# Performance work log

Measured on AMD Instinct MI355X. Metric: run time of the kernel, lower is better.

## Reference

```python
import jax, jax.numpy as jnp
import numpy as np

HEADS = 16
EPS = 1e-6


def _layernorm(x, gamma, beta):
    # LayerNorm over the last dim (per-head channel dim), eps=1e-6, affine.
    mu = jnp.mean(x, axis=-1, keepdims=True)
    var = jnp.mean(jnp.square(x - mu), axis=-1, keepdims=True)
    return (x - mu) * jax.lax.rsqrt(var + EPS) * gamma + beta


def setup_inputs() -> dict:
    key = jax.random.key(0)
    k_qkv, = jax.random.split(key, 1)
    bs, n_ctx, width3 = 1, 4096, 3072  # packed qkv: 3 * model_width (model_width=1024)
    attn_ch = width3 // HEADS // 3     # 64
    qkv = jax.random.normal(k_qkv, (bs, n_ctx, width3), dtype=jnp.float32)
    return {
        "qkv": qkv,
        "q_gamma": jnp.ones((attn_ch,), dtype=jnp.float32),
        "q_beta": jnp.zeros((attn_ch,), dtype=jnp.float32),
        "k_gamma": jnp.ones((attn_ch,), dtype=jnp.float32),
        "k_beta": jnp.zeros((attn_ch,), dtype=jnp.float32),
    }


def reference(qkv, q_gamma, q_beta, k_gamma, k_beta):
    bs, n_ctx, width3 = qkv.shape
    attn_ch = width3 // HEADS // 3
    # scale applied to both q and k -> total 1/sqrt(attn_ch)
    scale = 1.0 / np.sqrt(np.sqrt(attn_ch))
    qkv = qkv.reshape(bs, n_ctx, HEADS, 3 * attn_ch)
    q, k, v = jnp.split(qkv, 3, axis=-1)  # each [b, n, h, c]
    q = _layernorm(q, q_gamma, q_beta)
    k = _layernorm(k, k_gamma, k_beta)
    # manual (flash=False) path: einsum -> fp32 softmax -> einsum
    weight = jnp.einsum('bthc,bshc->bhts', q * scale, k * scale)
    wdtype = weight.dtype
    weight = jax.nn.softmax(weight.astype(jnp.float32), axis=-1).astype(wdtype)
    out = jnp.einsum('bhts,bshc->bthc', weight, v).reshape(bs, n_ctx, HEADS * attn_ch)
    return out
```

## Files before the change

### kernel.cpp

```cpp
#include <hip/hip_runtime.h>
#include <math.h>

#define TCTX 4096
#define HEADS 16
#define W3 3072
#define BQ 128
#define BK 64
#define NT 512
#define LSTR 65
#define HSTR 72

typedef short bf16x8 __attribute__((ext_vector_type(8)));
typedef float f32x4 __attribute__((ext_vector_type(4)));

static __device__ __forceinline__ unsigned short f2bf(float x) {
    union { float f; unsigned int u; } v; v.f = x;
    unsigned int r = v.u + 0x7fffu + ((v.u >> 16) & 1u);
    return (unsigned short)(r >> 16);
}
static __device__ __forceinline__ float bf2f(unsigned short h) {
    union { float f; unsigned int u; } v; v.u = ((unsigned int)h) << 16;
    return v.f;
}
#define PK2(a,b) ((unsigned int)(a) | ((unsigned int)(b) << 16))

__global__ __launch_bounds__(NT, 1) void attn_r17_kernel(
    const float* __restrict__ qkv,
    const float* __restrict__ q_gamma, const float* __restrict__ q_beta,
    const float* __restrict__ k_gamma, const float* __restrict__ k_beta,
    float* __restrict__ out)
{
    __shared__ float Ss[BQ * LSTR];
    __shared__ unsigned short Qh[BQ * HSTR], Ql[BQ * HSTR];
    __shared__ unsigned short Kh[BK * HSTR], Kl[BK * HSTR];
    __shared__ unsigned short Vth[64 * HSTR], Vtl[64 * HSTR];
    __shared__ unsigned short Ph[BQ * HSTR], Pl[BQ * HSTR];
    __shared__ float axs[BQ];
    __shared__ float lin[BQ];

    const int tid  = threadIdx.x;
    const int h    = blockIdx.y;
    const int q0   = blockIdx.x * BQ;
    const int lane = tid & 63;
    const int wv   = tid >> 6;
    const int l15  = lane & 15;
    const int quad = lane >> 4;
    const int m0   = wv * 16;
    const int r    = tid >> 2;
    const int j    = tid & 3;

    const float scale = 0.35355339059327373f;

    {
        const float* qp = qkv + (size_t)(q0 + r) * W3 + h * 192 + j * 16;
        f32x4 x0 = *(const f32x4*)(qp);
        f32x4 x1 = *(const f32x4*)(qp + 4);
        f32x4 x2 = *(const f32x4*)(qp + 8);
        f32x4 x3 = *(const f32x4*)(qp + 12);
        float s = 0.f, s2 = 0.f;
        #pragma unroll
        for (int i = 0; i < 16; ++i) {
            float x = (i < 4 ? x0[i & 3] : i < 8 ? x1[i & 3] : i < 12 ? x2[i & 3] : x3[i & 3]);
            s += x; s2 += x * x;
        }
        s  += __shfl_xor(s, 1);  s  += __shfl_xor(s, 2);
        s2 += __shfl_xor(s2, 1); s2 += __shfl_xor(s2, 2);
        float mu   = s * (1.f / 64.f);
        float var  = s2 * (1.f / 64.f) - mu * mu;
        float rsig = rsqrtf(var + 1e-6f);
        unsigned short hi[16], lo[16];
        #pragma unroll
        for (int i = 0; i < 16; ++i) {
            int c = j * 16 + i;
            float x = (i < 4 ? x0[i & 3] : i < 8 ? x1[i & 3] : i < 12 ? x2[i & 3] : x3[i & 3]);
            float y = ((x - mu) * rsig * q_gamma[c] + q_beta[c]) * scale;
            unsigned short yh = f2bf(y);
            hi[i] = yh;
            lo[i] = f2bf(y - bf2f(yh));
        }
        uint4* dh = (uint4*)(Qh + r * HSTR + j * 16);
        dh[0] = make_uint4(PK2(hi[0],hi[1]), PK2(hi[2],hi[3]), PK2(hi[4],hi[5]), PK2(hi[6],hi[7]));
        dh[1] = make_uint4(PK2(hi[8],hi[9]), PK2(hi[10],hi[11]), PK2(hi[12],hi[13]), PK2(hi[14],hi[15]));
        uint4* dl = (uint4*)(Ql + r * HSTR + j * 16);
        dl[0] = make_uint4(PK2(lo[0],lo[1]), PK2(lo[2],lo[3]), PK2(lo[4],lo[5]), PK2(lo[6],lo[7]));
        dl[1] = make_uint4(PK2(lo[8],lo[9]), PK2(lo[10],lo[11]), PK2(lo[12],lo[13]), PK2(lo[14],lo[15]));
    }
    __syncthreads();

    bf16x8 qh0 = *(const bf16x8*)(Qh + (m0 + l15) * HSTR +      quad * 8);
    bf16x8 qh1 = *(const bf16x8*)(Qh + (m0 + l15) * HSTR + 32 + quad * 8);
    bf16x8 ql0 = *(const bf16x8*)(Ql + (m0 + l15) * HSTR +      quad * 8);
    bf16x8 ql1 = *(const bf16x8*)(Ql + (m0 + l15) * HSTR + 32 + quad * 8);

    float m = -1e30f;
    float l = 0.f;
    f32x4 acco[4];
    #pragma unroll
    for (int t = 0; t < 4; ++t) acco[t] = (f32x4){0.f, 0.f, 0.f, 0.f};

    f32x4 kq0, kq1, kq2, kq3;
    float4 vv0, vv1, vv2, vv3;
    if (tid < 256) {
        const float* kp = qkv + (size_t)(0 + r) * W3 + h * 192 + 64 + j * 16;
        kq0 = *(const f32x4*)(kp);
        kq1 = *(const f32x4*)(kp + 4);
        kq2 = *(const f32x4*)(kp + 8);
        kq3 = *(const f32x4*)(kp + 12);
    } else {
        const int r2 = r - 64;
        const float4* src = (const float4*)(qkv + (size_t)(0 + r2) * W3 + h * 192 + 128 + j * 16);
        vv0 = src[0]; vv1 = src[1]; vv2 = src[2]; vv3 = src[3];
    }

    for (int s0 = 0; s0 < TCTX; s0 += BK) {
        __syncthreads();

        if (tid < 256) {
            float s = 0.f, s2 = 0.f;
            #pragma unroll
            for (int i = 0; i < 16; ++i) {
                float x = (i < 4 ? kq0[i & 3] : i < 8 ? kq1[i & 3] : i < 12 ? kq2[i & 3] : kq3[i & 3]);
                s += x; s2 += x * x;
            }
            s  += __shfl_xor(s, 1);  s  += __shfl_xor(s, 2);
            s2 += __shfl_xor(s2, 1); s2 += __shfl_xor(s2, 2);
            float mu   = s * (1.f / 64.f);
            float var  = s2 * (1.f / 64.f) - mu * mu;
            float rsig = rsqrtf(var + 1e-6f);
            unsigned short hi[16], lo[16];
            #pragma unroll
            for (int i = 0; i < 16; ++i) {
                int c = j * 16 + i;
                float x = (i < 4 ? kq0[i & 3] : i < 8 ? kq1[i & 3] : i < 12 ? kq2[i & 3] : kq3[i & 3]);
                float y = ((x - mu) * rsig * k_gamma[c] + k_beta[c]) * scale;
                unsigned short yh = f2bf(y);
                hi[i] = yh;
                lo[i] = f2bf(y - bf2f(yh));
            }
            uint4* dh = (uint4*)(Kh + r * HSTR + j * 16);
            dh[0] = make_uint4(PK2(hi[0],hi[1]), PK2(hi[2],hi[3]), PK2(hi[4],hi[5]), PK2(hi[6],hi[7]));
            dh[1] = make_uint4(PK2(hi[8],hi[9]), PK2(hi[10],hi[11]), PK2(hi[12],hi[13]), PK2(hi[14],hi[15]));
            uint4* dl = (uint4*)(Kl + r * HSTR + j * 16);
            dl[0] = make_uint4(PK2(lo[0],lo[1]), PK2(lo[2],lo[3]), PK2(lo[4],lo[5]), PK2(lo[6],lo[7]));
            dl[1] = make_uint4(PK2(lo[8],lo[9]), PK2(lo[10],lo[11]), PK2(lo[12],lo[13]), PK2(lo[14],lo[15]));
        } else {
            const int r2 = r - 64;
            #pragma unroll
            for (int c = 0; c < 4; ++c) {
                float4 v4 = (c == 0 ? vv0 : c == 1 ? vv1 : c == 2 ? vv2 : vv3);
                float vvv[4] = {v4.x, v4.y, v4.z, v4.w};
                #pragma unroll
                for (int k = 0; k < 4; ++k) {
                    unsigned short vh = f2bf(vvv[k]);
                    Vth[(j*16 + 4*c + k) * HSTR + r2] = vh;
                    Vtl[(j*16 + 4*c + k) * HSTR + r2] = f2bf(vvv[k] - bf2f(vh));
                }
            }
        }
        __syncthreads();

        {
            f32x4 accs[4];
            #pragma unroll
            for (int t = 0; t < 4; ++t) accs[t] = (f32x4){0.f, 0.f, 0.f, 0.f};
            #pragma unroll
            for (int s = 0; s < 2; ++s) {
                bf16x8 qh = s ? qh1 : qh0;
                bf16x8 ql = s ? ql1 : ql0;
                #pragma unroll
                for (int t = 0; t < 4; ++t) {
                    bf16x8 kh = *(const bf16x8*)(Kh + (t*16 + l15) * HSTR + s*32 + quad*8);
                    bf16x8 kl = *(const bf16x8*)(Kl + (t*16 + l15) * HSTR + s*32 + quad*8);
                    accs[t] = __builtin_amdgcn_mfma_f32_16x16x32_bf16(ql, kh, accs[t], 0, 0, 0);
                    accs[t] = __builtin_amdgcn_mfma_f32_16x16x32_bf16(qh, kl, accs[t], 0, 0, 0);
                    accs[t] = __builtin_amdgcn_mfma_f32_16x16x32_bf16(qh, kh, accs[t], 0, 0, 0);
                }
            }
            #pragma unroll
            for (int t = 0; t < 4; ++t)
                #pragma unroll
                for (int i = 0; i < 4; ++i)
                    Ss[(m0 + quad*4 + i) * LSTR + t*16 + l15] = accs[t][i];
        }
        __syncthreads();

        {
            float sv[16];
            for (int i = 0; i < 16; ++i)
                sv[i] = Ss[r * LSTR + j * 16 + i];

            float tmax = sv[0];
            for (int i = 1; i < 16; ++i) tmax = fmaxf(tmax, sv[i]);
            tmax = fmaxf(tmax, __shfl_xor(tmax, 1));
            tmax = fmaxf(tmax, __shfl_xor(tmax, 2));
            float new_m = fmaxf(m, tmax);
            float alpha = __expf(m - new_m);
            float psum = 0.f;
            unsigned short hi[16], lo[16];
            for (int i = 0; i < 16; ++i) {
                float p = __expf(sv[i] - new_m);
                psum += p;
                unsigned short ph = f2bf(p);
                hi[i] = ph;
                lo[i] = f2bf(p - bf2f(ph));
            }
            psum += __shfl_xor(psum, 1);
            psum += __shfl_xor(psum, 2);
            l = l * alpha + psum;
            m = new_m;
            uint4* dh = (uint4*)(Ph + r * HSTR + j * 16);
            dh[0] = make_uint4(PK2(hi[0],hi[1]), PK2(hi[2],hi[3]), PK2(hi[4],hi[5]), PK2(hi[6],hi[7]));
            dh[1] = make_uint4(PK2(hi[8],hi[9]), PK2(hi[10],hi[11]), PK2(hi[12],hi[13]), PK2(hi[14],hi[15]));
            uint4* dl = (uint4*)(Pl + r * HSTR + j * 16);
            dl[0] = make_uint4(PK2(lo[0],lo[1]), PK2(lo[2],lo[3]), PK2(lo[4],lo[5]), PK2(lo[6],lo[7]));
            dl[1] = make_uint4(PK2(lo[8],lo[9]), PK2(lo[10],lo[11]), PK2(lo[12],lo[13]), PK2(lo[14],lo[15]));
            if (j == 0) axs[r] = alpha;
        }
        __syncthreads();

        {
            float af[4];
            #pragma unroll
            for (int i = 0; i < 4; ++i) af[i] = axs[m0 + quad*4 + i];
            #pragma unroll
            for (int t = 0; t < 4; ++t)
                #pragma unroll
                for (int i = 0; i < 4; ++i)
                    acco[t][i] *= af[i];
        }

        if (s0 + BK < TCTX) {
            const int sn = s0 + BK;
            if (tid < 256) {
                const float* kp = qkv + (size_t)(sn + r) * W3 + h * 192 + 64 + j * 16;
                kq0 = *(const f32x4*)(kp);
                kq1 = *(const f32x4*)(kp + 4);
                kq2 = *(const f32x4*)(kp + 8);
                kq3 = *(const f32x4*)(kp + 12);
            } else {
                const int r2 = r - 64;
                const float4* src = (const float4*)(qkv + (size_t)(sn + r2) * W3 + h * 192 + 128 + j * 16);
                vv0 = src[0]; vv1 = src[1]; vv2 = src[2]; vv3 = src[3];
            }
        }

        #pragma unroll
        for (int s = 0; s < 2; ++s) {
            bf16x8 pa_h = *(const bf16x8*)(Ph + (m0 + l15) * HSTR + s*32 + quad*8);
            bf16x8 pa_l = *(const bf16x8*)(Pl + (m0 + l15) * HSTR + s*32 + quad*8);
            #pragma unroll
            for (int t = 0; t < 4; ++t) {
                bf16x8 vb_h = *(const bf16x8*)(Vth + (t*16 + l15) * HSTR + s*32 + quad*8);
                bf16x8 vb_l = *(const bf16x8*)(Vtl + (t*16 + l15) * HSTR + s*32 + quad*8);
                acco[t] = __builtin_amdgcn_mfma_f32_16x16x32_bf16(pa_l, vb_h, acco[t], 0, 0, 0);
                acco[t] = __builtin_amdgcn_mfma_f32_16x16x32_bf16(pa_h, vb_l, acco[t], 0, 0, 0);
                acco[t] = __builtin_amdgcn_mfma_f32_16x16x32_bf16(pa_h, vb_h, acco[t], 0, 0, 0);
            }
        }
    }

    if (j == 0) lin[r] = 1.f / l;
    __syncthreads();
    {
        float il[4];
        #pragma unroll
        for (int i = 0; i < 4; ++i) il[i] = lin[m0 + quad*4 + i];
        #pragma unroll
        for (int i = 0; i < 4; ++i) {
            const int row = q0 + m0 + quad*4 + i;
            float* op = out + (size_t)row * (HEADS * 64) + h * 64 + l15;
            #pragma unroll
            for (int t = 0; t < 4; ++t)
                op[t * 16] = acco[t][i] * il[i];
        }
    }
}

extern "C" void kernel_launch(void* const* d_in, const int* in_sizes, int n_in,
                              void* d_out, int out_size, void* d_ws, size_t ws_size,
                              hipStream_t stream) {
    const float* qkv     = (const float*)d_in[0];
    const float* q_gamma = (const float*)d_in[1];
    const float* q_beta  = (const float*)d_in[2];
    const float* k_gamma = (const float*)d_in[3];
    const float* k_beta  = (const float*)d_in[4];
    float* out = (float*)d_out;

    dim3 grid(TCTX / BQ, HEADS);
    attn_r17_kernel<<<grid, NT, 0, stream>>>(qkv, q_gamma, q_beta,
                                             k_gamma, k_beta, out);
}
```

Measured before the change: 510.7 us.

## Compute online softmax directly on MFMA accumulator registers, drop score LDS round-trip

```diff
diff --git a/kernel.cpp b/kernel.cpp
--- a/kernel.cpp
+++ b/kernel.cpp
@@ -7,7 +7,6 @@
 #define BQ 128
 #define BK 64
 #define NT 512
-#define LSTR 65
 #define HSTR 72
 
 typedef short bf16x8 __attribute__((ext_vector_type(8)));
@@ -24,19 +23,16 @@
 }
 #define PK2(a,b) ((unsigned int)(a) | ((unsigned int)(b) << 16))
 
-__global__ __launch_bounds__(NT, 1) void attn_r17_kernel(
+__global__ __launch_bounds__(NT, 1) void attn_r18_kernel(
     const float* __restrict__ qkv,
     const float* __restrict__ q_gamma, const float* __restrict__ q_beta,
     const float* __restrict__ k_gamma, const float* __restrict__ k_beta,
     float* __restrict__ out)
 {
-    __shared__ float Ss[BQ * LSTR];
     __shared__ unsigned short Qh[BQ * HSTR], Ql[BQ * HSTR];
     __shared__ unsigned short Kh[BK * HSTR], Kl[BK * HSTR];
     __shared__ unsigned short Vth[64 * HSTR], Vtl[64 * HSTR];
     __shared__ unsigned short Ph[BQ * HSTR], Pl[BQ * HSTR];
-    __shared__ float axs[BQ];
-    __shared__ float lin[BQ];
 
     const int tid  = threadIdx.x;
     const int h    = blockIdx.y;
@@ -92,8 +88,9 @@
     bf16x8 ql0 = *(const bf16x8*)(Ql + (m0 + l15) * HSTR +      quad * 8);
     bf16x8 ql1 = *(const bf16x8*)(Ql + (m0 + l15) * HSTR + 32 + quad * 8);
 
-    float m = -1e30f;
-    float l = 0.f;
+    float mreg[4], lreg[4];
+    #pragma unroll
+    for (int i = 0; i < 4; ++i) { mreg[i] = -1e30f; lreg[i] = 0.f; }
     f32x4 acco[4];
     #pragma unroll
     for (int t = 0; t < 4; ++t) acco[t] = (f32x4){0.f, 0.f, 0.f, 0.f};
@@ -159,75 +156,63 @@
         }
         __syncthreads();
 
-        {
-            f32x4 accs[4];
-            #pragma unroll
-            for (int t = 0; t < 4; ++t) accs[t] = (f32x4){0.f, 0.f, 0.f, 0.f};
-            #pragma unroll
-            for (int s = 0; s < 2; ++s) {
-                bf16x8 qh = s ? qh1 : qh0;
-                bf16x8 ql = s ? ql1 : ql0;
-                #pragma unroll
-                for (int t = 0; t < 4; ++t) {
-                    bf16x8 kh = *(const bf16x8*)(Kh + (t*16 + l15) * HSTR + s*32 + quad*8);
-                    bf16x8 kl = *(const bf16x8*)(Kl + (t*16 + l15) * HSTR + s*32 + quad*8);
-                    accs[t] = __builtin_amdgcn_mfma_f32_16x16x32_bf16(ql, kh, accs[t], 0, 0, 0);
-                    accs[t] = __builtin_amdgcn_mfma_f32_16x16x32_bf16(qh, kl, accs[t], 0, 0, 0);
-                    accs[t] = __builtin_amdgcn_mfma_f32_16x16x32_bf16(qh, kh, accs[t], 0, 0, 0);
-                }
-            }
-            #pragma unroll
-            for (int t = 0; t < 4; ++t)
-                #pragma unroll
-                for (int i = 0; i < 4; ++i)
-                    Ss[(m0 + quad*4 + i) * LSTR + t*16 + l15] = accs[t][i];
+        f32x4 accs[4];
+        #pragma unroll
+        for (int t = 0; t < 4; ++t) accs[t] = (f32x4){0.f, 0.f, 0.f, 0.f};
+        #pragma unroll
+        for (int s = 0; s < 2; ++s) {
+            bf16x8 qh = s ? qh1 : qh0;
+            bf16x8 ql = s ? ql1 : ql0;
+            #pragma unroll
+            for (int t = 0; t < 4; ++t) {
+                bf16x8 kh = *(const bf16x8*)(Kh + (t*16 + l15) * HSTR + s*32 + quad*8);
+                bf16x8 kl = *(const bf16x8*)(Kl + (t*16 + l15) * HSTR + s*32 + quad*8);
+                accs[t] = __builtin_amdgcn_mfma_f32_16x16x32_bf16(ql, kh, accs[t], 0, 0, 0);
+                accs[t] = __builtin_amdgcn_mfma_f32_16x16x32_bf16(qh, kl, accs[t], 0, 0, 0);
+                accs[t] = __builtin_amdgcn_mfma_f32_16x16x32_bf16(qh, kh, accs[t], 0, 0, 0);
+            }
+        }
+
+        float alpha[4];
+        #pragma unroll
+        for (int i = 0; i < 4; ++i) {
+            float mx = fmaxf(fmaxf(accs[0][i], accs[1][i]), fmaxf(accs[2][i], accs[3][i]));
+            mx = fmaxf(mx, __shfl_xor(mx, 1));
+            mx = fmaxf(mx, __shfl_xor(mx, 2));
+            mx = fmaxf(mx, __shfl_xor(mx, 4));
+            mx = fmaxf(mx, __shfl_xor(mx, 8));
+            float new_m = fmaxf(mreg[i], mx);
+            alpha[i] = __expf(mreg[i] - new_m);
+            mreg[i]  = new_m;
+        }
+        float ps[4] = {0.f, 0.f, 0.f, 0.f};
+        #pragma unroll
+        for (int t = 0; t < 4; ++t) {
+            #pragma unroll
+            for (int i = 0; i < 4; ++i) {
+                float p = __expf(accs[t][i] - mreg[i]);
+                ps[i] += p;
+                unsigned short ph = f2bf(p);
+                const int row = m0 + quad * 4 + i;
+                Ph[row * HSTR + t * 16 + l15] = ph;
+                Pl[row * HSTR + t * 16 + l15] = f2bf(p - bf2f(ph));
+            }
+        }
+        #pragma unroll
+        for (int i = 0; i < 4; ++i) {
+            ps[i] += __shfl_xor(ps[i], 1);
+            ps[i] += __shfl_xor(ps[i], 2);
+            ps[i] += __shfl_xor(ps[i], 4);
+            ps[i] += __shfl_xor(ps[i], 8);
+            lreg[i] = lreg[i] * alpha[i] + ps[i];
         }
         __syncthreads();
 
-        {
-            float sv[16];
-            for (int i = 0; i < 16; ++i)
-                sv[i] = Ss[r * LSTR + j * 16 + i];
-
-            float tmax = sv[0];
-            for (int i = 1; i < 16; ++i) tmax = fmaxf(tmax, sv[i]);
-            tmax = fmaxf(tmax, __shfl_xor(tmax, 1));
-            tmax = fmaxf(tmax, __shfl_xor(tmax, 2));
-            float new_m = fmaxf(m, tmax);
-            float alpha = __expf(m - new_m);
-            float psum = 0.f;
-            unsigned short hi[16], lo[16];
-            for (int i = 0; i < 16; ++i) {
-                float p = __expf(sv[i] - new_m);
-                psum += p;
-                unsigned short ph = f2bf(p);
-                hi[i] = ph;
-                lo[i] = f2bf(p - bf2f(ph));
-            }
-            psum += __shfl_xor(psum, 1);
-            psum += __shfl_xor(psum, 2);
-            l = l * alpha + psum;
-            m = new_m;
-            uint4* dh = (uint4*)(Ph + r * HSTR + j * 16);
-            dh[0] = make_uint4(PK2(hi[0],hi[1]), PK2(hi[2],hi[3]), PK2(hi[4],hi[5]), PK2(hi[6],hi[7]));
-            dh[1] = make_uint4(PK2(hi[8],hi[9]), PK2(hi[10],hi[11]), PK2(hi[12],hi[13]), PK2(hi[14],hi[15]));
-            uint4* dl = (uint4*)(Pl + r * HSTR + j * 16);
-            dl[0] = make_uint4(PK2(lo[0],lo[1]), PK2(lo[2],lo[3]), PK2(lo[4],lo[5]), PK2(lo[6],lo[7]));
-            dl[1] = make_uint4(PK2(lo[8],lo[9]), PK2(lo[10],lo[11]), PK2(lo[12],lo[13]), PK2(lo[14],lo[15]));
-            if (j == 0) axs[r] = alpha;
-        }
-        __syncthreads();
-
-        {
-            float af[4];
-            #pragma unroll
-            for (int i = 0; i < 4; ++i) af[i] = axs[m0 + quad*4 + i];
-            #pragma unroll
-            for (int t = 0; t < 4; ++t)
-                #pragma unroll
-                for (int i = 0; i < 4; ++i)
-                    acco[t][i] *= af[i];
-        }
+        #pragma unroll
+        for (int t = 0; t < 4; ++t)
+            #pragma unroll
+            for (int i = 0; i < 4; ++i)
+                acco[t][i] *= alpha[i];
 
         if (s0 + BK < TCTX) {
             const int sn = s0 + BK;
@@ -259,20 +244,14 @@
         }
     }
 
-    if (j == 0) lin[r] = 1.f / l;
-    __syncthreads();
-    {
-        float il[4];
-        #pragma unroll
-        for (int i = 0; i < 4; ++i) il[i] = lin[m0 + quad*4 + i];
-        #pragma unroll
-        for (int i = 0; i < 4; ++i) {
-            const int row = q0 + m0 + quad*4 + i;
-            float* op = out + (size_t)row * (HEADS * 64) + h * 64 + l15;
-            #pragma unroll
-            for (int t = 0; t < 4; ++t)
-                op[t * 16] = acco[t][i] * il[i];
-        }
+    #pragma unroll
+    for (int i = 0; i < 4; ++i) {
+        const float il = 1.f / lreg[i];
+        const int row = q0 + m0 + quad * 4 + i;
+        float* op = out + (size_t)row * (HEADS * 64) + h * 64 + l15;
+        #pragma unroll
+        for (int t = 0; t < 4; ++t)
+            op[t * 16] = acco[t][i] * il;
     }
 }
 
@@ -287,6 +266,6 @@
     float* out = (float*)d_out;
 
     dim3 grid(TCTX / BQ, HEADS);
-    attn_r17_kernel<<<grid, NT, 0, stream>>>(qkv, q_gamma, q_beta,
+    attn_r18_kernel<<<grid, NT, 0, stream>>>(qkv, q_gamma, q_beta,
                                              k_gamma, k_beta, out);
 }
```

Result: slower. 522.8 us (+2.4%).
